# Kernel optimization log

Measured on AMD Instinct MI355X. Metric: run time of the kernel, lower is better.

## Reference

```python
import jax, jax.numpy as jnp
import numpy as np

JITTER_NOISE = 0.01


def setup_inputs() -> dict:
    key = jax.random.key(0)
    k1, k2, k3 = jax.random.split(key, 3)
    B, S, H, E = 8, 4096, 2048, 64
    token_inputs = jax.random.normal(k1, (B, S, H), dtype=jnp.float32)
    # multiplicative jitter in [1 - eps, 1 + eps]
    jitter = jax.random.uniform(k2, (B, S, H), dtype=jnp.float32,
                                minval=1.0 - JITTER_NOISE, maxval=1.0 + JITTER_NOISE)
    w = jax.random.normal(k3, (H, E), dtype=jnp.float32) * 0.02
    b = jnp.zeros((E,), dtype=jnp.float32)
    return {"token_inputs": token_inputs, "jitter": jitter, "w": w, "b": b,
            "num_experts": E, "top_k": 2}


def reference(token_inputs, jitter, w, b, num_experts, top_k):
    # float32 routing computation with jitter noise
    x = token_inputs.astype(jnp.float32) * jitter
    # router logits: [B, S, E]
    logits = jnp.einsum('bsh,he->bse', x, w) + b
    probs = jax.nn.softmax(logits, axis=-1)  # [B, S, E]
    # top-k one-hot mask over experts
    top_k_indices = jax.lax.top_k(probs, top_k)[1]          # [B, S, K]
    mask = jax.nn.one_hot(top_k_indices, num_experts,
                          dtype=jnp.float32).sum(axis=-2)    # [B, S, E]
    return probs * mask
```

## Files before the change

### kernel.cpp

```cpp
#include <hip/hip_runtime.h>


#define H   2048
#define E   64

typedef __attribute__((ext_vector_type(8))) short bf16x8;
typedef __attribute__((ext_vector_type(4))) float f32x4;

__device__ inline ushort f2bf_rne(float f) {
    union { float f; unsigned u; } c; c.f = f;
    const unsigned r = (c.u + 0x7FFFu + ((c.u >> 16) & 1u)) >> 16;
    return (ushort)r;
}
__device__ inline float bf2f(ushort h) {
    union { unsigned u; float f; } c; c.u = ((unsigned)h) << 16;
    return c.f;
}

__global__ __launch_bounds__(256)
void wpack_kernel(const float* __restrict__ w, ushort* __restrict__ bp)
{
    const int t    = blockIdx.x * 256 + threadIdx.x;
    const int lane = t & 63;
    const int n    = (t >> 6) & 3;
    const int ks   = t >> 8;
    const int c    = lane & 15, g = lane >> 4;

    const float* src = w + (size_t)(ks * 32 + g * 8) * E + n * 16 + c;
    bf16x8 vh, vl;
#pragma unroll
    for (int s = 0; s < 8; ++s) {
        const float  v = src[(size_t)s * E];
        const ushort h = f2bf_rne(v);
        vh[s] = (short)h;
        vl[s] = (short)f2bf_rne(v - bf2f(h));
    }
    ushort* d = bp + ((size_t)(ks * 4 + n) * 2 * 64 + lane) * 8;
    *(bf16x8*)d         = vh;
    *(bf16x8*)(d + 512) = vl;
}

__global__ __launch_bounds__(256, 4)
void router_kernel(const float* __restrict__ xg,
                   const float* __restrict__ jg,
                   const ushort* __restrict__ bp,
                   const float* __restrict__ bias,
                   float* __restrict__ out)
{
    __shared__ float lgx[4][16][68];

    const int tid  = threadIdx.x;
    const int wv   = tid >> 6;
    const int lane = tid & 63;
    const int ln   = lane & 15;
    const int g    = lane >> 4;
    const size_t tokBase = (size_t)blockIdx.x * 16;

    const float* xp = xg + (tokBase + ln) * (size_t)H + wv * 512 + g * 8;
    const float* jp = jg + (tokBase + ln) * (size_t)H + wv * 512 + g * 8;
    const ushort* bpw = bp + (size_t)(wv * 16) * 4096 + (size_t)lane * 8;

    f32x4 acc0 = (f32x4){0.f, 0.f, 0.f, 0.f};
    f32x4 acc1 = (f32x4){0.f, 0.f, 0.f, 0.f};
    f32x4 acc2 = (f32x4){0.f, 0.f, 0.f, 0.f};
    f32x4 acc3 = (f32x4){0.f, 0.f, 0.f, 0.f};

#pragma unroll 2
    for (int ks = 0; ks < 16; ++ks) {
        const float* xq = xp + ks * 32;
        const float* jq = jp + ks * 32;
        const float4 x0 = *(const float4*)(xq);
        const float4 x1 = *(const float4*)(xq + 4);
        const float4 j0 = *(const float4*)(jq);
        const float4 j1 = *(const float4*)(jq + 4);

        float pr[8];
        pr[0] = x0.x * j0.x; pr[1] = x0.y * j0.y;
        pr[2] = x0.z * j0.z; pr[3] = x0.w * j0.w;
        pr[4] = x1.x * j1.x; pr[5] = x1.y * j1.y;
        pr[6] = x1.z * j1.z; pr[7] = x1.w * j1.w;

        bf16x8 ah, al;
#pragma unroll
        for (int i = 0; i < 8; ++i) {
            const ushort h = f2bf_rne(pr[i]);
            ah[i] = (short)h;
            al[i] = (short)f2bf_rne(pr[i] - bf2f(h));
        }

        const ushort* bq = bpw + (size_t)ks * 4096;
        {
            const bf16x8 BH = *(const bf16x8*)(bq);
            const bf16x8 BL = *(const bf16x8*)(bq + 512);
            acc0 = __builtin_amdgcn_mfma_f32_16x16x32_bf16(ah, BH, acc0, 0, 0, 0);
            acc0 = __builtin_amdgcn_mfma_f32_16x16x32_bf16(al, BH, acc0, 0, 0, 0);
            acc0 = __builtin_amdgcn_mfma_f32_16x16x32_bf16(ah, BL, acc0, 0, 0, 0);
        }
        {
            const bf16x8 BH = *(const bf16x8*)(bq + 1024);
            const bf16x8 BL = *(const bf16x8*)(bq + 1536);
            acc1 = __builtin_amdgcn_mfma_f32_16x16x32_bf16(ah, BH, acc1, 0, 0, 0);
            acc1 = __builtin_amdgcn_mfma_f32_16x16x32_bf16(al, BH, acc1, 0, 0, 0);
            acc1 = __builtin_amdgcn_mfma_f32_16x16x32_bf16(ah, BL, acc1, 0, 0, 0);
        }
        {
            const bf16x8 BH = *(const bf16x8*)(bq + 2048);
            const bf16x8 BL = *(const bf16x8*)(bq + 2560);
            acc2 = __builtin_amdgcn_mfma_f32_16x16x32_bf16(ah, BH, acc2, 0, 0, 0);
            acc2 = __builtin_amdgcn_mfma_f32_16x16x32_bf16(al, BH, acc2, 0, 0, 0);
            acc2 = __builtin_amdgcn_mfma_f32_16x16x32_bf16(ah, BL, acc2, 0, 0, 0);
        }
        {
            const bf16x8 BH = *(const bf16x8*)(bq + 3072);
            const bf16x8 BL = *(const bf16x8*)(bq + 3584);
            acc3 = __builtin_amdgcn_mfma_f32_16x16x32_bf16(ah, BH, acc3, 0, 0, 0);
            acc3 = __builtin_amdgcn_mfma_f32_16x16x32_bf16(al, BH, acc3, 0, 0, 0);
            acc3 = __builtin_amdgcn_mfma_f32_16x16x32_bf16(ah, BL, acc3, 0, 0, 0);
        }
    }

#pragma unroll
    for (int r = 0; r < 4; ++r) {
        lgx[wv][g * 4 + r][     ln] = acc0[r];
        lgx[wv][g * 4 + r][16 + ln] = acc1[r];
        lgx[wv][g * 4 + r][32 + ln] = acc2[r];
        lgx[wv][g * 4 + r][48 + ln] = acc3[r];
    }
    __syncthreads();

    if (tid < 128) {
        const int t8 = tid >> 3;
        const int q8 = tid & 7;
        const int eb = q8 * 8;

        float l[8];
        {
            const float4 a0 = *(const float4*)&lgx[0][t8][eb];
            const float4 a1 = *(const float4*)&lgx[1][t8][eb];
            const float4 a2 = *(const float4*)&lgx[2][t8][eb];
            const float4 a3 = *(const float4*)&lgx[3][t8][eb];
            const float4 b0 = *(const float4*)&lgx[0][t8][eb + 4];
            const float4 b1 = *(const float4*)&lgx[1][t8][eb + 4];
            const float4 b2 = *(const float4*)&lgx[2][t8][eb + 4];
            const float4 b3 = *(const float4*)&lgx[3][t8][eb + 4];
            const float4 bb0 = *(const float4*)(bias + eb);
            const float4 bb1 = *(const float4*)(bias + eb + 4);
            l[0] = a0.x + a1.x + a2.x + a3.x + bb0.x;
            l[1] = a0.y + a1.y + a2.y + a3.y + bb0.y;
            l[2] = a0.z + a1.z + a2.z + a3.z + bb0.z;
            l[3] = a0.w + a1.w + a2.w + a3.w + bb0.w;
            l[4] = b0.x + b1.x + b2.x + b3.x + bb1.x;
            l[5] = b0.y + b1.y + b2.y + b3.y + bb1.y;
            l[6] = b0.z + b1.z + b2.z + b3.z + bb1.z;
            l[7] = b0.w + b1.w + b2.w + b3.w + bb1.w;
        }

        float p1 = l[0]; int i1 = eb;
        float p2 = -3.0e38f; int i2 = eb;
#pragma unroll
        for (int i = 1; i < 8; ++i) {
            const int e = eb + i;
            if (l[i] > p1)      { p2 = p1; i2 = i1; p1 = l[i]; i1 = e; }
            else if (l[i] > p2) { p2 = l[i]; i2 = e; }
        }

#pragma unroll
        for (int m = 1; m <= 4; m <<= 1) {
            const float q1 = __shfl_xor(p1, m, 8);
            const int   k1 = __shfl_xor(i1, m, 8);
            const float q2 = __shfl_xor(p2, m, 8);
            const int   k2 = __shfl_xor(i2, m, 8);
            const bool  bw = (q1 > p1) || (q1 == p1 && k1 < i1);
            const float f1 = bw ? q1 : p1;  const int fi1 = bw ? k1 : i1;
            const float lo = bw ? p1 : q1;  const int loi = bw ? i1 : k1;
            const float sn = bw ? q2 : p2;  const int sni = bw ? k2 : i2;
            const bool  rw = (lo > sn) || (lo == sn && loi < sni);
            p2 = rw ? lo : sn;  i2 = rw ? loi : sni;
            p1 = f1;            i1 = fi1;
        }

        float d = 0.f;
#pragma unroll
        for (int i = 0; i < 8; ++i) d += __expf(l[i] - p1);
#pragma unroll
        for (int m = 1; m <= 4; m <<= 1) d += __shfl_xor(d, m, 8);

        const float inv = 1.f / d;
        const float w2  = __expf(p2 - p1) * inv;

        float* op = out + (tokBase + t8) * (size_t)E + eb;
        float4 v0, v1;
        v0.x = (eb + 0 == i1) ? inv : (eb + 0 == i2) ? w2 : 0.f;
        v0.y = (eb + 1 == i1) ? inv : (eb + 1 == i2) ? w2 : 0.f;
        v0.z = (eb + 2 == i1) ? inv : (eb + 2 == i2) ? w2 : 0.f;
        v0.w = (eb + 3 == i1) ? inv : (eb + 3 == i2) ? w2 : 0.f;
        v1.x = (eb + 4 == i1) ? inv : (eb + 4 == i2) ? w2 : 0.f;
        v1.y = (eb + 5 == i1) ? inv : (eb + 5 == i2) ? w2 : 0.f;
        v1.z = (eb + 6 == i1) ? inv : (eb + 6 == i2) ? w2 : 0.f;
        v1.w = (eb + 7 == i1) ? inv : (eb + 7 == i2) ? w2 : 0.f;
        *(float4*)op       = v0;
        *(float4*)(op + 4) = v1;
    }
}

extern "C" void kernel_launch(void* const* d_in, const int* in_sizes, int n_in,
                              void* d_out, int out_size, void* d_ws, size_t ws_size,
                              hipStream_t stream)
{
    const float* x   = (const float*)d_in[0];
    const float* jit = (const float*)d_in[1];
    const float* w   = (const float*)d_in[2];
    const float* b   = (const float*)d_in[3];
    float*       out = (float*)d_out;

    ushort* bpack = (ushort*)d_ws;

    hipLaunchKernelGGL(wpack_kernel, dim3(64), dim3(256), 0, stream, w, bpack);

    const int n_tok = in_sizes[0] / H;
    dim3 grid(n_tok / 16), block(256);
    hipLaunchKernelGGL(router_kernel, grid, block, 0, stream,
                       x, jit, bpack, b, out);
}
```

Measured before the change: 147.9 us.

## Stage split-bf16 activations through swizzled LDS with coalesced row loads, 32 tokens per block

Each block now handles 32 tokens, with waves split two ways over tokens and two ways over K. Each wave loads contiguous 1 KB row segments of x and jitter with 8 loads issued ahead. It converts the product to hi/lo bf16 and writes it into an XOR-swizzled LDS buffer, then reads MFMA A-fragments back from it. This replaces the strided per-lane float4 loads with better-coalesced wide row reads and halves per-block weight traffic relative to tokens. In exchange it uses 64 KB of LDS, which limits occupancy to about 2 blocks per CU, and adds an LDS round trip.

```diff
diff --git a/kernel.cpp b/kernel.cpp
--- a/kernel.cpp
+++ b/kernel.cpp
@@ -7,13 +7,12 @@
 typedef __attribute__((ext_vector_type(8))) short bf16x8;
 typedef __attribute__((ext_vector_type(4))) float f32x4;
 
-__device__ inline ushort f2bf_rne(float f) {
+__device__ inline unsigned bfhi(float f) {
     union { float f; unsigned u; } c; c.f = f;
-    const unsigned r = (c.u + 0x7FFFu + ((c.u >> 16) & 1u)) >> 16;
-    return (ushort)r;
-}
-__device__ inline float bf2f(ushort h) {
-    union { unsigned u; float f; } c; c.u = ((unsigned)h) << 16;
+    return (c.u + 0x7FFFu + ((c.u >> 16) & 1u)) >> 16;
+}
+__device__ inline float bf2f(unsigned h) {
+    union { unsigned u; float f; } c; c.u = h << 16;
     return c.f;
 }
 
@@ -30,177 +29,197 @@
     bf16x8 vh, vl;
 #pragma unroll
     for (int s = 0; s < 8; ++s) {
-        const float  v = src[(size_t)s * E];
-        const ushort h = f2bf_rne(v);
+        const float v = src[(size_t)s * E];
+        const unsigned h = bfhi(v);
         vh[s] = (short)h;
-        vl[s] = (short)f2bf_rne(v - bf2f(h));
+        vl[s] = (short)bfhi(v - bf2f(h));
     }
     ushort* d = bp + ((size_t)(ks * 4 + n) * 2 * 64 + lane) * 8;
     *(bf16x8*)d         = vh;
     *(bf16x8*)(d + 512) = vl;
 }
 
-__global__ __launch_bounds__(256, 4)
+__global__ __launch_bounds__(256, 2)
 void router_kernel(const float* __restrict__ xg,
                    const float* __restrict__ jg,
                    const ushort* __restrict__ bp,
                    const float* __restrict__ bias,
                    float* __restrict__ out)
 {
-    __shared__ float lgx[4][16][68];
+    __shared__ __align__(16) unsigned char arena[65536];
 
     const int tid  = threadIdx.x;
     const int wv   = tid >> 6;
     const int lane = tid & 63;
-    const int ln   = lane & 15;
+    const int tc   = lane & 15;
     const int g    = lane >> 4;
-    const size_t tokBase = (size_t)blockIdx.x * 16;
-
-    const float* xp = xg + (tokBase + ln) * (size_t)H + wv * 512 + g * 8;
-    const float* jp = jg + (tokBase + ln) * (size_t)H + wv * 512 + g * 8;
-    const ushort* bpw = bp + (size_t)(wv * 16) * 4096 + (size_t)lane * 8;
+    const int th   = wv & 1;
+    const int kh   = wv >> 1;
+    const size_t tokBase = (size_t)blockIdx.x * 32;
+    const size_t rowBase = tokBase + th * 16;
+
+    ushort* hiP = (ushort*)(arena + wv * 16384);
+    ushort* loP = hiP + 4096;
+
+    const ushort* bpw = bp + (size_t)lane * 8;
 
     f32x4 acc0 = (f32x4){0.f, 0.f, 0.f, 0.f};
     f32x4 acc1 = (f32x4){0.f, 0.f, 0.f, 0.f};
     f32x4 acc2 = (f32x4){0.f, 0.f, 0.f, 0.f};
     f32x4 acc3 = (f32x4){0.f, 0.f, 0.f, 0.f};
 
-#pragma unroll 2
-    for (int ks = 0; ks < 16; ++ks) {
-        const float* xq = xp + ks * 32;
-        const float* jq = jp + ks * 32;
-        const float4 x0 = *(const float4*)(xq);
-        const float4 x1 = *(const float4*)(xq + 4);
-        const float4 j0 = *(const float4*)(jq);
-        const float4 j1 = *(const float4*)(jq + 4);
-
-        float pr[8];
-        pr[0] = x0.x * j0.x; pr[1] = x0.y * j0.y;
-        pr[2] = x0.z * j0.z; pr[3] = x0.w * j0.w;
-        pr[4] = x1.x * j1.x; pr[5] = x1.y * j1.y;
-        pr[6] = x1.z * j1.z; pr[7] = x1.w * j1.w;
-
-        bf16x8 ah, al;
-#pragma unroll
-        for (int i = 0; i < 8; ++i) {
-            const ushort h = f2bf_rne(pr[i]);
-            ah[i] = (short)h;
-            al[i] = (short)f2bf_rne(pr[i] - bf2f(h));
+    const int wgr  = lane >> 1;
+    const int whf  = (lane & 1) * 4;
+
+#pragma unroll 1
+    for (int cc = 0; cc < 4; ++cc) {
+        const size_t kb = (size_t)kh * 1024 + (size_t)cc * 256 + lane * 4;
+
+#pragma unroll
+        for (int grp = 0; grp < 2; ++grp) {
+            float4 xr[8], jr[8];
+#pragma unroll
+            for (int i = 0; i < 8; ++i) {
+                const size_t row = rowBase + grp * 8 + i;
+                xr[i] = *(const float4*)(xg + row * H + kb);
+                jr[i] = *(const float4*)(jg + row * H + kb);
+            }
+            __builtin_amdgcn_sched_barrier(0);
+#pragma unroll
+            for (int i = 0; i < 8; ++i) {
+                const int ri = grp * 8 + i;
+                const float p0 = xr[i].x * jr[i].x;
+                const float p1 = xr[i].y * jr[i].y;
+                const float p2 = xr[i].z * jr[i].z;
+                const float p3 = xr[i].w * jr[i].w;
+                const unsigned h0 = bfhi(p0), h1 = bfhi(p1);
+                const unsigned h2 = bfhi(p2), h3 = bfhi(p3);
+                const unsigned l0 = bfhi(p0 - bf2f(h0));
+                const unsigned l1 = bfhi(p1 - bf2f(h1));
+                const unsigned l2 = bfhi(p2 - bf2f(h2));
+                const unsigned l3 = bfhi(p3 - bf2f(h3));
+                const int idx = ri * 256 + ((wgr ^ (ri & 7)) << 3) + whf;
+                uint2 hv; hv.x = h0 | (h1 << 16); hv.y = h2 | (h3 << 16);
+                uint2 lv; lv.x = l0 | (l1 << 16); lv.y = l2 | (l3 << 16);
+                *(uint2*)&hiP[idx] = hv;
+                *(uint2*)&loP[idx] = lv;
+            }
         }
 
-        const ushort* bq = bpw + (size_t)ks * 4096;
-        {
-            const bf16x8 BH = *(const bf16x8*)(bq);
-            const bf16x8 BL = *(const bf16x8*)(bq + 512);
-            acc0 = __builtin_amdgcn_mfma_f32_16x16x32_bf16(ah, BH, acc0, 0, 0, 0);
-            acc0 = __builtin_amdgcn_mfma_f32_16x16x32_bf16(al, BH, acc0, 0, 0, 0);
-            acc0 = __builtin_amdgcn_mfma_f32_16x16x32_bf16(ah, BL, acc0, 0, 0, 0);
+#pragma unroll
+        for (int ks = 0; ks < 8; ++ks) {
+            const int rg  = ((ks * 4 + g) ^ (tc & 7)) << 3;
+            const bf16x8 ah = *(const bf16x8*)&hiP[tc * 256 + rg];
+            const bf16x8 al = *(const bf16x8*)&loP[tc * 256 + rg];
+
+            const int gks = kh * 32 + cc * 8 + ks;
+            const ushort* bq = bpw + (size_t)gks * 4096;
+            {
+                const bf16x8 BH = *(const bf16x8*)(bq);
+                const bf16x8 BL = *(const bf16x8*)(bq + 512);
+                acc0 = __builtin_amdgcn_mfma_f32_16x16x32_bf16(ah, BH, acc0, 0, 0, 0);
+                acc0 = __builtin_amdgcn_mfma_f32_16x16x32_bf16(al, BH, acc0, 0, 0, 0);
+                acc0 = __builtin_amdgcn_mfma_f32_16x16x32_bf16(ah, BL, acc0, 0, 0, 0);
+            }
+            {
+                const bf16x8 BH = *(const bf16x8*)(bq + 1024);
+                const bf16x8 BL = *(const bf16x8*)(bq + 1536);
+                acc1 = __builtin_amdgcn_mfma_f32_16x16x32_bf16(ah, BH, acc1, 0, 0, 0);
+                acc1 = __builtin_amdgcn_mfma_f32_16x16x32_bf16(al, BH, acc1, 0, 0, 0);
+                acc1 = __builtin_amdgcn_mfma_f32_16x16x32_bf16(ah, BL, acc1, 0, 0, 0);
+            }
+            {
+                const bf16x8 BH = *(const bf16x8*)(bq + 2048);
+                const bf16x8 BL = *(const bf16x8*)(bq + 2560);
+                acc2 = __builtin_amdgcn_mfma_f32_16x16x32_bf16(ah, BH, acc2, 0, 0, 0);
+                acc2 = __builtin_amdgcn_mfma_f32_16x16x32_bf16(al, BH, acc2, 0, 0, 0);
+                acc2 = __builtin_amdgcn_mfma_f32_16x16x32_bf16(ah, BL, acc2, 0, 0, 0);
+            }
+            {
+                const bf16x8 BH = *(const bf16x8*)(bq + 3072);
+                const bf16x8 BL = *(const bf16x8*)(bq + 3584);
+                acc3 = __builtin_amdgcn_mfma_f32_16x16x32_bf16(ah, BH, acc3, 0, 0, 0);
+                acc3 = __builtin_amdgcn_mfma_f32_16x16x32_bf16(al, BH, acc3, 0, 0, 0);
+                acc3 = __builtin_amdgcn_mfma_f32_16x16x32_bf16(ah, BL, acc3, 0, 0, 0);
+            }
         }
-        {
-            const bf16x8 BH = *(const bf16x8*)(bq + 1024);
-            const bf16x8 BL = *(const bf16x8*)(bq + 1536);
-            acc1 = __builtin_amdgcn_mfma_f32_16x16x32_bf16(ah, BH, acc1, 0, 0, 0);
-            acc1 = __builtin_amdgcn_mfma_f32_16x16x32_bf16(al, BH, acc1, 0, 0, 0);
-            acc1 = __builtin_amdgcn_mfma_f32_16x16x32_bf16(ah, BL, acc1, 0, 0, 0);
-        }
-        {
-            const bf16x8 BH = *(const bf16x8*)(bq + 2048);
-            const bf16x8 BL = *(const bf16x8*)(bq + 2560);
-            acc2 = __builtin_amdgcn_mfma_f32_16x16x32_bf16(ah, BH, acc2, 0, 0, 0);
-            acc2 = __builtin_amdgcn_mfma_f32_16x16x32_bf16(al, BH, acc2, 0, 0, 0);
-            acc2 = __builtin_amdgcn_mfma_f32_16x16x32_bf16(ah, BL, acc2, 0, 0, 0);
-        }
-        {
-            const bf16x8 BH = *(const bf16x8*)(bq + 3072);
-            const bf16x8 BL = *(const bf16x8*)(bq + 3584);
-            acc3 = __builtin_amdgcn_mfma_f32_16x16x32_bf16(ah, BH, acc3, 0, 0, 0);
-            acc3 = __builtin_amdgcn_mfma_f32_16x16x32_bf16(al, BH, acc3, 0, 0, 0);
-            acc3 = __builtin_amdgcn_mfma_f32_16x16x32_bf16(ah, BL, acc3, 0, 0, 0);
-        }
-    }
-
+    }
+
+    __syncthreads();
+    float (*lgx)[32][68] = (float (*)[32][68])(void*)arena;
 #pragma unroll
     for (int r = 0; r < 4; ++r) {
-        lgx[wv][g * 4 + r][     ln] = acc0[r];
-        lgx[wv][g * 4 + r][16 + ln] = acc1[r];
-        lgx[wv][g * 4 + r][32 + ln] = acc2[r];
-        lgx[wv][g * 4 + r][48 + ln] = acc3[r];
+        const int trow = th * 16 + g * 4 + r;
+        lgx[kh][trow][     tc] = acc0[r];
+        lgx[kh][trow][16 + tc] = acc1[r];
+        lgx[kh][trow][32 + tc] = acc2[r];
+        lgx[kh][trow][48 + tc] = acc3[r];
     }
     __syncthreads();
 
-    if (tid < 128) {
-        const int t8 = tid >> 3;
-        const int q8 = tid & 7;
-        const int eb = q8 * 8;
-
-        float l[8];
-        {
-            const float4 a0 = *(const float4*)&lgx[0][t8][eb];
-            const float4 a1 = *(const float4*)&lgx[1][t8][eb];
-            const float4 a2 = *(const float4*)&lgx[2][t8][eb];
-            const float4 a3 = *(const float4*)&lgx[3][t8][eb];
-            const float4 b0 = *(const float4*)&lgx[0][t8][eb + 4];
-            const float4 b1 = *(const float4*)&lgx[1][t8][eb + 4];
-            const float4 b2 = *(const float4*)&lgx[2][t8][eb + 4];
-            const float4 b3 = *(const float4*)&lgx[3][t8][eb + 4];
-            const float4 bb0 = *(const float4*)(bias + eb);
-            const float4 bb1 = *(const float4*)(bias + eb + 4);
-            l[0] = a0.x + a1.x + a2.x + a3.x + bb0.x;
-            l[1] = a0.y + a1.y + a2.y + a3.y + bb0.y;
-            l[2] = a0.z + a1.z + a2.z + a3.z + bb0.z;
-            l[3] = a0.w + a1.w + a2.w + a3.w + bb0.w;
-            l[4] = b0.x + b1.x + b2.x + b3.x + bb1.x;
-            l[5] = b0.y + b1.y + b2.y + b3.y + bb1.y;
-            l[6] = b0.z + b1.z + b2.z + b3.z + bb1.z;
-            l[7] = b0.w + b1.w + b2.w + b3.w + bb1.w;
-        }
-
-        float p1 = l[0]; int i1 = eb;
-        float p2 = -3.0e38f; int i2 = eb;
-#pragma unroll
-        for (int i = 1; i < 8; ++i) {
-            const int e = eb + i;
-            if (l[i] > p1)      { p2 = p1; i2 = i1; p1 = l[i]; i1 = e; }
-            else if (l[i] > p2) { p2 = l[i]; i2 = e; }
-        }
-
-#pragma unroll
-        for (int m = 1; m <= 4; m <<= 1) {
-            const float q1 = __shfl_xor(p1, m, 8);
-            const int   k1 = __shfl_xor(i1, m, 8);
-            const float q2 = __shfl_xor(p2, m, 8);
-            const int   k2 = __shfl_xor(i2, m, 8);
-            const bool  bw = (q1 > p1) || (q1 == p1 && k1 < i1);
-            const float f1 = bw ? q1 : p1;  const int fi1 = bw ? k1 : i1;
-            const float lo = bw ? p1 : q1;  const int loi = bw ? i1 : k1;
-            const float sn = bw ? q2 : p2;  const int sni = bw ? k2 : i2;
-            const bool  rw = (lo > sn) || (lo == sn && loi < sni);
-            p2 = rw ? lo : sn;  i2 = rw ? loi : sni;
-            p1 = f1;            i1 = fi1;
-        }
-
-        float d = 0.f;
-#pragma unroll
-        for (int i = 0; i < 8; ++i) d += __expf(l[i] - p1);
-#pragma unroll
-        for (int m = 1; m <= 4; m <<= 1) d += __shfl_xor(d, m, 8);
-
-        const float inv = 1.f / d;
-        const float w2  = __expf(p2 - p1) * inv;
-
-        float* op = out + (tokBase + t8) * (size_t)E + eb;
-        float4 v0, v1;
-        v0.x = (eb + 0 == i1) ? inv : (eb + 0 == i2) ? w2 : 0.f;
-        v0.y = (eb + 1 == i1) ? inv : (eb + 1 == i2) ? w2 : 0.f;
-        v0.z = (eb + 2 == i1) ? inv : (eb + 2 == i2) ? w2 : 0.f;
-        v0.w = (eb + 3 == i1) ? inv : (eb + 3 == i2) ? w2 : 0.f;
-        v1.x = (eb + 4 == i1) ? inv : (eb + 4 == i2) ? w2 : 0.f;
-        v1.y = (eb + 5 == i1) ? inv : (eb + 5 == i2) ? w2 : 0.f;
-        v1.z = (eb + 6 == i1) ? inv : (eb + 6 == i2) ? w2 : 0.f;
-        v1.w = (eb + 7 == i1) ? inv : (eb + 7 == i2) ? w2 : 0.f;
-        *(float4*)op       = v0;
-        *(float4*)(op + 4) = v1;
-    }
+    const int t8 = tid >> 3;
+    const int q8 = tid & 7;
+    const int eb = q8 * 8;
+
+    float l[8];
+    {
+        const float4 a0 = *(const float4*)&lgx[0][t8][eb];
+        const float4 a1 = *(const float4*)&lgx[1][t8][eb];
+        const float4 b0 = *(const float4*)&lgx[0][t8][eb + 4];
+        const float4 b1 = *(const float4*)&lgx[1][t8][eb + 4];
+        const float4 bb0 = *(const float4*)(bias + eb);
+        const float4 bb1 = *(const float4*)(bias + eb + 4);
+        l[0] = a0.x + a1.x + bb0.x;  l[1] = a0.y + a1.y + bb0.y;
+        l[2] = a0.z + a1.z + bb0.z;  l[3] = a0.w + a1.w + bb0.w;
+        l[4] = b0.x + b1.x + bb1.x;  l[5] = b0.y + b1.y + bb1.y;
+        l[6] = b0.z + b1.z + bb1.z;  l[7] = b0.w + b1.w + bb1.w;
+    }
+
+    float p1 = l[0]; int i1 = eb;
+    float p2 = -3.0e38f; int i2 = eb;
+#pragma unroll
+    for (int i = 1; i < 8; ++i) {
+        const int e = eb + i;
+        if (l[i] > p1)      { p2 = p1; i2 = i1; p1 = l[i]; i1 = e; }
+        else if (l[i] > p2) { p2 = l[i]; i2 = e; }
+    }
+
+#pragma unroll
+    for (int m = 1; m <= 4; m <<= 1) {
+        const float q1 = __shfl_xor(p1, m, 8);
+        const int   k1 = __shfl_xor(i1, m, 8);
+        const float q2 = __shfl_xor(p2, m, 8);
+        const int   k2 = __shfl_xor(i2, m, 8);
+        const bool  bw = (q1 > p1) || (q1 == p1 && k1 < i1);
+        const float f1 = bw ? q1 : p1;  const int fi1 = bw ? k1 : i1;
+        const float lo = bw ? p1 : q1;  const int loi = bw ? i1 : k1;
+        const float sn = bw ? q2 : p2;  const int sni = bw ? k2 : i2;
+        const bool  rw = (lo > sn) || (lo == sn && loi < sni);
+        p2 = rw ? lo : sn;  i2 = rw ? loi : sni;
+        p1 = f1;            i1 = fi1;
+    }
+
+    float d = 0.f;
+#pragma unroll
+    for (int i = 0; i < 8; ++i) d += __expf(l[i] - p1);
+#pragma unroll
+    for (int m = 1; m <= 4; m <<= 1) d += __shfl_xor(d, m, 8);
+
+    const float inv = 1.f / d;
+    const float w2  = __expf(p2 - p1) * inv;
+
+    float* op = out + (tokBase + t8) * (size_t)E + eb;
+    float4 v0, v1;
+    v0.x = (eb + 0 == i1) ? inv : (eb + 0 == i2) ? w2 : 0.f;
+    v0.y = (eb + 1 == i1) ? inv : (eb + 1 == i2) ? w2 : 0.f;
+    v0.z = (eb + 2 == i1) ? inv : (eb + 2 == i2) ? w2 : 0.f;
+    v0.w = (eb + 3 == i1) ? inv : (eb + 3 == i2) ? w2 : 0.f;
+    v1.x = (eb + 4 == i1) ? inv : (eb + 4 == i2) ? w2 : 0.f;
+    v1.y = (eb + 5 == i1) ? inv : (eb + 5 == i2) ? w2 : 0.f;
+    v1.z = (eb + 6 == i1) ? inv : (eb + 6 == i2) ? w2 : 0.f;
+    v1.w = (eb + 7 == i1) ? inv : (eb + 7 == i2) ? w2 : 0.f;
+    *(float4*)op       = v0;
+    *(float4*)(op + 4) = v1;
 }
 
 extern "C" void kernel_launch(void* const* d_in, const int* in_sizes, int n_in,
@@ -218,7 +237,7 @@
     hipLaunchKernelGGL(wpack_kernel, dim3(64), dim3(256), 0, stream, w, bpack);
 
     const int n_tok = in_sizes[0] / H;
-    dim3 grid(n_tok / 16), block(256);
+    dim3 grid(n_tok / 32), block(256);
     hipLaunchKernelGGL(router_kernel, grid, block, 0, stream,
                        x, jit, bpack, b, out);
 }
```

New measurement: 157.4 us. 1.06x slower.
